# Performance work log

Hardware: AMD Instinct MI355X
Metric: run time of the kernel (lower is better)

## Reference

```python
import jax, jax.numpy as jnp
import numpy as np

STRIDE = 1
PADDING = 1
DILATION = 1


def setup_inputs() -> dict:
    key = jax.random.key(0)
    k1, k2, k3 = jax.random.split(key, 3)
    x = jax.random.normal(k1, (32, 18, 256, 256), dtype=jnp.float32)
    # DeformConv2d weight layout: [out_channels, in_channels, kh, kw]
    weight = jax.random.normal(k2, (64, 18, 3, 3), dtype=jnp.float32) * 0.1
    bias = jax.random.normal(k3, (64,), dtype=jnp.float32) * 0.1
    return {"x": x, "weight": weight, "bias": bias}


def reference(x, weight, bias):
    # offset = zeros_like(x): all sampling offsets are exactly zero, so the
    # bilinear sampling in deformable conv hits integer grid points and the
    # op is mathematically identical to a standard conv2d.
    out = jax.lax.conv_general_dilated(
        x, weight,
        window_strides=(STRIDE, STRIDE),
        padding=[(PADDING, PADDING), (PADDING, PADDING)],
        rhs_dilation=(DILATION, DILATION),
        dimension_numbers=("NCHW", "OIHW", "NCHW"),
    )
    return out + bias[None, :, None, None]
```

## Files before the change

kernel.cpp:

```cpp
#include <hip/hip_runtime.h>


#define N_  32
#define IC_ 18
#define H_  256
#define W_  256
#define OC_ 64
#define KW_TOT (IC_ * 9)

__global__ __launch_bounds__(256, 3)
void conv3x3_kernel(const float* __restrict__ x,
                    const float* __restrict__ wgt,
                    const float* __restrict__ bias,
                    float* __restrict__ out) {
    __shared__ float wS[KW_TOT * OC_];

    const int tid = threadIdx.x;

    for (int i = tid; i < KW_TOT * OC_; i += 256) {
        const int k  = i >> 6;
        const int oc = i & 63;
        wS[i] = wgt[oc * KW_TOT + k];
    }
    __syncthreads();

    const int tx     = tid & 63;
    const int wv     = tid >> 6;
    const int ocBase = wv * 16;
    const int w0     = blockIdx.x * 64;
    const int h0     = blockIdx.y * 4;
    const int n      = blockIdx.z;

    float acc[4][16];
    #pragma unroll
    for (int o = 0; o < 16; ++o) {
        const float b = bias[ocBase + o];
        #pragma unroll
        for (int ty = 0; ty < 4; ++ty) acc[ty][o] = b;
    }

    const float* xn = x + (size_t)n * IC_ * H_ * W_;

    for (int ic = 0; ic < IC_; ++ic) {
        const float* xc = xn + ic * (H_ * W_);

        float xv[6][3];
        #pragma unroll
        for (int r = 0; r < 6; ++r) {
            const int gh = h0 - 1 + r;
            const bool rowOK = (unsigned)gh < (unsigned)H_;
            #pragma unroll
            for (int kw = 0; kw < 3; ++kw) {
                const int gw = w0 - 1 + tx + kw;
                const bool ok = rowOK && ((unsigned)gw < (unsigned)W_);
                xv[r][kw] = ok ? xc[gh * W_ + gw] : 0.0f;
            }
        }

        #pragma unroll
        for (int kh = 0; kh < 3; ++kh) {
            #pragma unroll
            for (int kw = 0; kw < 3; ++kw) {
                const float* wp = &wS[((ic * 3 + kh) * 3 + kw) * OC_ + ocBase];
                float wr[16];
                #pragma unroll
                for (int o = 0; o < 16; ++o) wr[o] = wp[o];
                #pragma unroll
                for (int ty = 0; ty < 4; ++ty) {
                    const float xs = xv[ty + kh][kw];
                    #pragma unroll
                    for (int o = 0; o < 16; ++o)
                        acc[ty][o] = fmaf(xs, wr[o], acc[ty][o]);
                }
            }
        }
    }

    #pragma unroll
    for (int o = 0; o < 16; ++o) {
        const int oc = ocBase + o;
        float* op = out + (((size_t)n * OC_ + oc) * H_ + h0) * (size_t)W_ + w0 + tx;
        #pragma unroll
        for (int ty = 0; ty < 4; ++ty)
            op[ty * W_] = acc[ty][o];
    }
}

extern "C" void kernel_launch(void* const* d_in, const int* in_sizes, int n_in,
                              void* d_out, int out_size, void* d_ws, size_t ws_size,
                              hipStream_t stream) {
    const float* x    = (const float*)d_in[0];
    const float* wgt  = (const float*)d_in[1];
    const float* bias = (const float*)d_in[2];
    float* out        = (float*)d_out;

    dim3 grid(W_ / 64, H_ / 4, N_);
    dim3 block(256);
    hipLaunchKernelGGL(conv3x3_kernel, grid, block, 0, stream,
                       x, wgt, bias, out);
}
```

Baseline: 1.357 ms.

## Chunk weights in LDS by input-channel halves and pre-transpose weights

Splits the input channels into two chunks of 9, so only half the weight tensor sits in shared memory at a time, halving LDS use and raising the occupancy hint from 3 to 6 blocks. A separate small kernel pre-transposes the weights into workspace so each block can copy them into LDS with contiguous float4 loads instead of a strided gather. In exchange it adds an extra launch and an extra barrier per chunk, and the higher occupancy target may squeeze registers for the 64 accumulators.

```diff
diff --git a/kernel.cpp b/kernel.cpp
--- a/kernel.cpp
+++ b/kernel.cpp
@@ -6,24 +6,30 @@
 #define H_  256
 #define W_  256
 #define OC_ 64
-#define KW_TOT (IC_ * 9)
+#define KTOT (IC_ * 9)
+#define ICC  9
+#define KCH  (ICC * 9)
+#define CHW  (KCH * OC_)
 
-__global__ __launch_bounds__(256, 3)
+__global__ __launch_bounds__(256)
+void transpose_w_kernel(const float* __restrict__ wgt, float* __restrict__ wT) {
+    const int i = blockIdx.x * 256 + threadIdx.x;
+    if (i < KTOT * OC_) {
+        const int k  = i >> 6;
+        const int oc = i & 63;
+        wT[i] = wgt[oc * KTOT + k];
+    }
+}
+
+template<bool TRANS>
+__global__ __launch_bounds__(256, 6)
 void conv3x3_kernel(const float* __restrict__ x,
-                    const float* __restrict__ wgt,
+                    const float* __restrict__ wsrc,
                     const float* __restrict__ bias,
                     float* __restrict__ out) {
-    __shared__ float wS[KW_TOT * OC_];
+    __shared__ float wS[CHW];
 
-    const int tid = threadIdx.x;
-
-    for (int i = tid; i < KW_TOT * OC_; i += 256) {
-        const int k  = i >> 6;
-        const int oc = i & 63;
-        wS[i] = wgt[oc * KW_TOT + k];
-    }
-    __syncthreads();
-
+    const int tid    = threadIdx.x;
     const int tx     = tid & 63;
     const int wv     = tid >> 6;
     const int ocBase = wv * 16;
@@ -41,36 +47,52 @@
 
     const float* xn = x + (size_t)n * IC_ * H_ * W_;
 
-    for (int ic = 0; ic < IC_; ++ic) {
-        const float* xc = xn + ic * (H_ * W_);
-
-        float xv[6][3];
-        #pragma unroll
-        for (int r = 0; r < 6; ++r) {
-            const int gh = h0 - 1 + r;
-            const bool rowOK = (unsigned)gh < (unsigned)H_;
-            #pragma unroll
-            for (int kw = 0; kw < 3; ++kw) {
-                const int gw = w0 - 1 + tx + kw;
-                const bool ok = rowOK && ((unsigned)gw < (unsigned)W_);
-                xv[r][kw] = ok ? xc[gh * W_ + gw] : 0.0f;
+    for (int c = 0; c < IC_ / ICC; ++c) {
+        __syncthreads();
+        if (TRANS) {
+            const float4* src = (const float4*)(wsrc + c * CHW);
+            float4*       dst = (float4*)wS;
+            for (int i = tid; i < CHW / 4; i += 256) dst[i] = src[i];
+        } else {
+            for (int i = tid; i < CHW; i += 256) {
+                const int k  = i >> 6;
+                const int oc = i & 63;
+                wS[i] = wsrc[oc * KTOT + c * KCH + k];
             }
         }
+        __syncthreads();
 
-        #pragma unroll
-        for (int kh = 0; kh < 3; ++kh) {
+        for (int ici = 0; ici < ICC; ++ici) {
+            const float* xc = xn + (c * ICC + ici) * (H_ * W_);
+
+            float xv[6][3];
             #pragma unroll
-            for (int kw = 0; kw < 3; ++kw) {
-                const float* wp = &wS[((ic * 3 + kh) * 3 + kw) * OC_ + ocBase];
-                float wr[16];
+            for (int r = 0; r < 6; ++r) {
+                const int gh = h0 - 1 + r;
+                const bool rowOK = (unsigned)gh < (unsigned)H_;
                 #pragma unroll
-                for (int o = 0; o < 16; ++o) wr[o] = wp[o];
+                for (int kw = 0; kw < 3; ++kw) {
+                    const int gw = w0 - 1 + tx + kw;
+                    const bool ok = rowOK && ((unsigned)gw < (unsigned)W_);
+                    xv[r][kw] = ok ? xc[gh * W_ + gw] : 0.0f;
+                }
+            }
+
+            #pragma unroll
+            for (int kh = 0; kh < 3; ++kh) {
                 #pragma unroll
-                for (int ty = 0; ty < 4; ++ty) {
-                    const float xs = xv[ty + kh][kw];
+                for (int kw = 0; kw < 3; ++kw) {
+                    const float* wp = &wS[((ici * 3 + kh) * 3 + kw) * OC_ + ocBase];
+                    float wr[16];
                     #pragma unroll
-                    for (int o = 0; o < 16; ++o)
-                        acc[ty][o] = fmaf(xs, wr[o], acc[ty][o]);
+                    for (int o = 0; o < 16; ++o) wr[o] = wp[o];
+                    #pragma unroll
+                    for (int ty = 0; ty < 4; ++ty) {
+                        const float xs = xv[ty + kh][kw];
+                        #pragma unroll
+                        for (int o = 0; o < 16; ++o)
+                            acc[ty][o] = fmaf(xs, wr[o], acc[ty][o]);
+                    }
                 }
             }
         }
@@ -94,8 +116,19 @@
     const float* bias = (const float*)d_in[2];
     float* out        = (float*)d_out;
 
+    const size_t wT_bytes = (size_t)KTOT * OC_ * sizeof(float);
     dim3 grid(W_ / 64, H_ / 4, N_);
     dim3 block(256);
-    hipLaunchKernelGGL(conv3x3_kernel, grid, block, 0, stream,
-                       x, wgt, bias, out);
+
+    if (d_ws != nullptr && ws_size >= wT_bytes) {
+        float* wT = (float*)d_ws;
+        hipLaunchKernelGGL(transpose_w_kernel,
+                           dim3((KTOT * OC_ + 255) / 256), block, 0, stream,
+                           wgt, wT);
+        hipLaunchKernelGGL(conv3x3_kernel<true>, grid, block, 0, stream,
+                           x, wT, bias, out);
+    } else {
+        hipLaunchKernelGGL(conv3x3_kernel<false>, grid, block, 0, stream,
+                           x, wgt, bias, out);
+    }
 }
```

New measurement: 4.809 ms. 254% more time.

## Retile conv to 8 rows x 4 channels per wave with scalar weight loads

Applied to the files above, without the earlier changes.

Drops the shared-memory weight staging and its barrier. Each wave now loads its own 4 output channels' weights directly with a wave-uniform base (readfirstlane), so the weights can sit in scalar registers. The output tile changes from 4 rows x 16 channels to 8 rows x 4 channels, and the grid splits output channels across blocks. Per-element column bounds checks become clamped indices with a select. Each input pixel is now loaded once per 16 output channels instead of 64, which raises global/L2 traffic for x, in exchange for fewer LDS reads, lower register pressure and more blocks.

```diff
diff --git a/kernel.cpp b/kernel.cpp
--- a/kernel.cpp
+++ b/kernel.cpp
@@ -6,54 +6,67 @@
 #define H_  256
 #define W_  256
 #define OC_ 64
-#define KW_TOT (IC_ * 9)
+#define HW_ (H_ * W_)
+#define KT_ (IC_ * 9)
 
 __global__ __launch_bounds__(256, 3)
 void conv3x3_kernel(const float* __restrict__ x,
                     const float* __restrict__ wgt,
                     const float* __restrict__ bias,
                     float* __restrict__ out) {
-    __shared__ float wS[KW_TOT * OC_];
+    const int tid = threadIdx.x;
+    const int tx  = tid & 63;
+    const int wv  = tid >> 6;
 
-    const int tid = threadIdx.x;
+    const int w0  = blockIdx.x * 64;
+    const int h0  = blockIdx.y * 8;
+    const int zz  = blockIdx.z;
+    const int n   = zz >> 2;
+    const int oc0 = __builtin_amdgcn_readfirstlane((zz & 3) * 16 + wv * 4);
 
-    for (int i = tid; i < KW_TOT * OC_; i += 256) {
-        const int k  = i >> 6;
-        const int oc = i & 63;
-        wS[i] = wgt[oc * KW_TOT + k];
-    }
-    __syncthreads();
+    const int  gwC = w0 + tx;
+    const bool okL = (gwC >= 1);
+    const bool okR = (gwC <= W_ - 2);
+    const int  gwL = okL ? gwC - 1 : 0;
+    const int  gwR = okR ? gwC + 1 : W_ - 1;
 
-    const int tx     = tid & 63;
-    const int wv     = tid >> 6;
-    const int ocBase = wv * 16;
-    const int w0     = blockIdx.x * 64;
-    const int h0     = blockIdx.y * 4;
-    const int n      = blockIdx.z;
-
-    float acc[4][16];
+    float acc[8][4];
     #pragma unroll
-    for (int o = 0; o < 16; ++o) {
-        const float b = bias[ocBase + o];
+    for (int o = 0; o < 4; ++o) {
+        const float b = bias[oc0 + o];
         #pragma unroll
-        for (int ty = 0; ty < 4; ++ty) acc[ty][o] = b;
+        for (int ty = 0; ty < 8; ++ty) acc[ty][o] = b;
     }
 
-    const float* xn = x + (size_t)n * IC_ * H_ * W_;
+    const float* xn = x + (size_t)n * IC_ * HW_;
 
+    #pragma unroll 1
     for (int ic = 0; ic < IC_; ++ic) {
-        const float* xc = xn + ic * (H_ * W_);
+        const float* wp = wgt + (size_t)oc0 * KT_ + ic * 9;
+        float wr[4][9];
+        #pragma unroll
+        for (int o = 0; o < 4; ++o) {
+            #pragma unroll
+            for (int t = 0; t < 9; ++t)
+                wr[o][t] = wp[o * KT_ + t];
+        }
 
-        float xv[6][3];
+        const float* xc = xn + (size_t)ic * HW_;
+
+        float xw[10][3];
         #pragma unroll
-        for (int r = 0; r < 6; ++r) {
+        for (int r = 0; r < 10; ++r) {
             const int gh = h0 - 1 + r;
-            const bool rowOK = (unsigned)gh < (unsigned)H_;
-            #pragma unroll
-            for (int kw = 0; kw < 3; ++kw) {
-                const int gw = w0 - 1 + tx + kw;
-                const bool ok = rowOK && ((unsigned)gw < (unsigned)W_);
-                xv[r][kw] = ok ? xc[gh * W_ + gw] : 0.0f;
+            if ((unsigned)gh < (unsigned)H_) {
+                const float* row = xc + gh * W_;
+                const float vL = row[gwL];
+                const float vC = row[gwC];
+                const float vR = row[gwR];
+                xw[r][0] = okL ? vL : 0.0f;
+                xw[r][1] = vC;
+                xw[r][2] = okR ? vR : 0.0f;
+            } else {
+                xw[r][0] = 0.0f; xw[r][1] = 0.0f; xw[r][2] = 0.0f;
             }
         }
 
@@ -61,28 +74,24 @@
         for (int kh = 0; kh < 3; ++kh) {
             #pragma unroll
             for (int kw = 0; kw < 3; ++kw) {
-                const float* wp = &wS[((ic * 3 + kh) * 3 + kw) * OC_ + ocBase];
-                float wr[16];
                 #pragma unroll
-                for (int o = 0; o < 16; ++o) wr[o] = wp[o];
-                #pragma unroll
-                for (int ty = 0; ty < 4; ++ty) {
-                    const float xs = xv[ty + kh][kw];
+                for (int ty = 0; ty < 8; ++ty) {
+                    const float xs = xw[ty + kh][kw];
                     #pragma unroll
-                    for (int o = 0; o < 16; ++o)
-                        acc[ty][o] = fmaf(xs, wr[o], acc[ty][o]);
+                    for (int o = 0; o < 4; ++o)
+                        acc[ty][o] = fmaf(xs, wr[o][kh * 3 + kw], acc[ty][o]);
                 }
             }
         }
     }
 
     #pragma unroll
-    for (int o = 0; o < 16; ++o) {
-        const int oc = ocBase + o;
-        float* op = out + (((size_t)n * OC_ + oc) * H_ + h0) * (size_t)W_ + w0 + tx;
+    for (int o = 0; o < 4; ++o) {
+        float* op = out + (((size_t)n * OC_ + (oc0 + o)) * H_ + h0) * (size_t)W_
+                  + w0 + tx;
         #pragma unroll
-        for (int ty = 0; ty < 4; ++ty)
-            op[ty * W_] = acc[ty][o];
+        for (int ty = 0; ty < 8; ++ty)
+            op[(size_t)ty * W_] = acc[ty][o];
     }
 }
 
@@ -94,7 +103,7 @@
     const float* bias = (const float*)d_in[2];
     float* out        = (float*)d_out;
 
-    dim3 grid(W_ / 64, H_ / 4, N_);
+    dim3 grid(W_ / 64, H_ / 8, N_ * 4);
     dim3 block(256);
     hipLaunchKernelGGL(conv3x3_kernel, grid, block, 0, stream,
                        x, wgt, bias, out);
```

After: 1.768 ms. 30.2% more time.
